# Kernel optimization log

Hardware: AMD Instinct MI355X
Metric: run time of the kernel (lower is better)

The kernel has to match this reference:

```python
import jax, jax.numpy as jnp
import numpy as np

NUM_BRANCH = 4
KERNEL_SIZES = (1, 3, 5, 7)
NUM_CLASSES = 1000
IN_C = 256
OUT_C = 256


def _cond_conv(x, w, emb, y):
    # x: [B,C,H,W], w: [O,I,k,k], emb: [num_classes,O], y: [B]
    out = jax.lax.conv_general_dilated(
        x, w, window_strides=(1, 1), padding='SAME',
        dimension_numbers=('NCHW', 'OIHW', 'NCHW'))
    return out + emb[y][:, :, None, None]


def setup_inputs() -> dict:
    key = jax.random.key(0)
    ks = jax.random.split(key, 2 + 2 * NUM_BRANCH)
    B, H = 64, 32
    inp = {
        'x': jax.random.normal(ks[0], (B, IN_C, H, H), dtype=jnp.float32),
        'y': jax.random.randint(ks[1], (B,), 0, NUM_CLASSES, dtype=jnp.int64),
        'sample_arc': jax.random.randint(jax.random.fold_in(key, 7), (B,), 0, NUM_BRANCH, dtype=jnp.int64),
    }
    for i, k in enumerate(KERNEL_SIZES):
        fan_in = IN_C * k * k
        inp[f'w{i}'] = jax.random.normal(ks[2 + 2 * i], (OUT_C, IN_C, k, k), dtype=jnp.float32) / np.sqrt(fan_in)
        inp[f'e{i}'] = jax.random.normal(ks[3 + 2 * i], (NUM_CLASSES, OUT_C), dtype=jnp.float32) * 0.02
    return inp


def reference(x, y, sample_arc, w0, w1, w2, w3, e0, e1, e2, e3):
    ws = (w0, w1, w2, w3)
    es = (e0, e1, e2, e3)
    # Compute every branch for every sample (as the original module does),
    # stack along branch dim: [B, num_branch, O, H, W]
    branch_out = jnp.stack([_cond_conv(x, w, e, y) for w, e in zip(ws, es)], axis=1)
    onehot = jax.nn.one_hot(sample_arc, NUM_BRANCH, dtype=x.dtype)  # [B, num_branch]
    # mask-and-sum (one-hot multiply then reduce over branch dim)
    return jnp.einsum('bn,bnchw->bchw', onehot, branch_out)
```

## Files before the change

### kernel.cpp

```cpp
#include <hip/hip_runtime.h>


typedef unsigned short ushort_t;
typedef __attribute__((ext_vector_type(8))) short short8;
typedef __attribute__((ext_vector_type(4))) float f32x4;

#define CIN   256
#define COUT  256
#define HH    32
#define WW    32
#define HW    1024

#define XT_ELEMS   16777216
#define WT_OFF_0   0
#define WT_OFF_1   65536
#define WT_OFF_2   655360
#define WT_OFF_3   2293760
#define WT_ELEMS   5505024
#define TILE_BYTE_OFF ((size_t)(XT_ELEMS + WT_ELEMS) * 2)
#define MAX_TILES  2048
#define WS_NEEDED  (TILE_BYTE_OFF + MAX_TILES * 2 + 64)

#define XS_R_STRIDE 1520
#define XS_C_STRIDE 40
#define XS_ELEMS    15200

__device__ inline ushort_t f2bf(float f) {
    unsigned x = __builtin_bit_cast(unsigned, f);
    unsigned r = (x + 0x7FFFu + ((x >> 16) & 1u)) >> 16;
    return (ushort_t)r;
}

__global__ __launch_bounds__(256) void prep_kernel(
    const float* __restrict__ x,
    const float* __restrict__ w0, const float* __restrict__ w1,
    const float* __restrict__ w2, const float* __restrict__ w3,
    const int* __restrict__ y, const int* __restrict__ arc,
    const float* __restrict__ e0, const float* __restrict__ e1,
    const float* __restrict__ e2, const float* __restrict__ e3,
    float* __restrict__ out,
    ushort_t* __restrict__ xt, ushort_t* __restrict__ wt,
    ushort_t* __restrict__ tiles, unsigned* __restrict__ cnt) {
    __shared__ float lds[2 * 32 * 49];
    const int blk = blockIdx.x;
    const int tid = threadIdx.x;

    if (blk < 4096) {
        const int a   = blk >> 10;
        const int cc  = (blk >> 7) & 7;
        const int oc0 = (blk & 127) * 2;
        const int kk  = (a == 0) ? 1 : (a == 1) ? 9 : (a == 2) ? 25 : 49;
        const float* __restrict__ w = (a == 0) ? w0 : (a == 1) ? w1
                                    : (a == 2) ? w2 : w3;
        const size_t woff = (a == 0) ? WT_OFF_0 : (a == 1) ? WT_OFF_1
                          : (a == 2) ? WT_OFF_2 : WT_OFF_3;
        const int ckk = 32 * kk;
#pragma unroll
        for (int ocq = 0; ocq < 2; ++ocq) {
            const float* src = w + ((size_t)((oc0 + ocq) * CIN + cc * 32)) * kk;
            for (int i = tid; i < ckk; i += 256) lds[ocq * ckk + i] = src[i];
        }
        __syncthreads();
        ushort_t* dst = wt + woff;
        const int F = 2 * kk * 32;
        for (int j = tid; j < F; j += 256) {
            const int ci  = j & 31;
            const int t2  = j >> 5;
            const int khw = t2 % kk;
            const int ocq = t2 / kk;
            dst[((size_t)(cc * kk + khw) * COUT + oc0 + ocq) * 32 + ci] =
                f2bf(lds[ocq * ckk + ci * kk + khw]);
        }
    } else if (blk < 6144) {
        const int id = (blk - 4096) * 256 + tid;
        const int hw = id & 1023;
        const int cc = (id >> 10) & 7;
        const int b  = id >> 13;
        const float* src = x + ((size_t)(b * CIN + cc * 32)) * HW + hw;
        ushort_t* dst = xt + ((size_t)((b * 8 + cc) * HW + hw)) * 32;
#pragma unroll
        for (int v = 0; v < 4; ++v) {
            short8 o;
#pragma unroll
            for (int j = 0; j < 8; ++j)
                o[j] = (short)f2bf(src[(size_t)(v * 8 + j) * HW]);
            *(short8*)(dst + v * 8) = o;
        }
    } else if (blk < 10240) {
        const int z   = blk - 6144;
        const int b   = z >> 6;
        const int oc  = (z & 63) * 4 + (tid >> 6);
        const int i   = tid & 63;
        const int a   = arc[b];
        const int cls = y[b];
        const float* __restrict__ e = (a == 0) ? e0 : (a == 1) ? e1
                                    : (a == 2) ? e2 : e3;
        const float ev = e[(size_t)cls * COUT + oc];
        float4 v = make_float4(ev, ev, ev, ev);
        float* ob = out + ((size_t)(b * COUT + oc)) * HW + i * 16;
#pragma unroll
        for (int k = 0; k < 4; ++k) *(float4*)(ob + k * 4) = v;
    } else if (tid < 64) {
        const int lane = tid;
        const int ab = (int)arc[lane];
        unsigned long long m[4];
#pragma unroll
        for (int v = 0; v < 4; ++v) m[v] = __ballot(ab == v);
        int gt = 0;
#pragma unroll
        for (int v = 1; v < 4; ++v) if (v > ab) gt += __popcll(m[v]);
        const unsigned long long eq = (ab == 0) ? m[0] : (ab == 1) ? m[1]
                                    : (ab == 2) ? m[2] : m[3];
        const unsigned long long lower = (lane == 0) ? 0ull
                                       : (~0ull >> (64 - lane));
        const int rank = gt + __popcll(eq & lower);
        const int nh   = __popcll(m[2]) + __popcll(m[3]);
        const bool heavy = (ab >= 2);
        const int myCnt = heavy ? 16 : 8;
        const int start = heavy ? 16 * rank : 16 * nh + 8 * (rank - nh);
        for (int j = 0; j < myCnt; ++j)
            tiles[start + j] = (ushort_t)((lane << 5) | j);
        if (lane == 0) { cnt[0] = 0u; cnt[1] = (unsigned)(512 + 8 * nh); }
    }
}

template <int K, int NCC, bool ATOMIC>
__device__ void conv_body(const ushort_t* __restrict__ xt,
                          const ushort_t* __restrict__ wtb,
                          const float* __restrict__ eb,
                          int b, int cls, int cc0, int r0,
                          float* __restrict__ out, ushort_t* xs) {
    constexpr int KK   = K * K;
    constexpr int PAD  = K / 2;
    constexpr int R    = 4 + 2 * PAD;
    constexpr int ITER = (R * 128) / 256;

    const int tid  = threadIdx.x;
    const int wave = tid >> 6;
    const int lane = tid & 63;
    const int wm   = wave;
    const int ln   = lane & 15;
    const int q    = lane >> 4;

    f32x4 acc[4][8];
#pragma unroll
    for (int mt = 0; mt < 4; ++mt)
#pragma unroll
        for (int nt = 0; nt < 8; ++nt) acc[mt][nt] = (f32x4)0.0f;

    constexpr size_t WSTEP = (size_t)COUT * 32;
    const ushort_t* wlane = wtb + ((size_t)(wm * 64 + ln)) * 32 + q * 8;
    short8 afp[4];
#pragma unroll
    for (int mt = 0; mt < 4; ++mt)
        afp[mt] = *(const short8*)&wlane[(size_t)(cc0 * KK) * WSTEP
                                         + (size_t)mt * 512];

    const ushort_t* xsrc = xt + ((size_t)b * 8) * (HW * 32);

    for (int cc2 = 0; cc2 < NCC; ++cc2) {
        const int cc = cc0 + cc2;
        __syncthreads();
#pragma unroll
        for (int i = 0; i < ITER; ++i) {
            const int id = tid + i * 256;
            const int r  = id >> 7;
            const int gw = (id >> 2) & 31;
            const int g4 = id & 3;
            const int gr = r0 - PAD + r;
            short8 v = (short8)0;
            if (gr >= 0 && gr < HH)
                v = *(const short8*)&xsrc[((size_t)(cc * HW + gr * WW + gw)) * 32 + g4 * 8];
            *(short8*)&xs[r * XS_R_STRIDE + (gw + 3) * XS_C_STRIDE + g4 * 8] = v;
        }
        __syncthreads();

#pragma unroll 1
        for (int kh = 0; kh < K; ++kh) {
#pragma unroll
            for (int kw = 0; kw < K; ++kw) {
                const int khw = kh * K + kw;
                const int idx = cc * KK + khw;
                short8 afc[4];
#pragma unroll
                for (int mt = 0; mt < 4; ++mt) afc[mt] = afp[mt];
                {
                    int nidx = idx + 1;
                    if (nidx == (cc0 + NCC) * KK) nidx = cc0 * KK;
                    const ushort_t* nb = wlane + (size_t)nidx * WSTEP;
#pragma unroll
                    for (int mt = 0; mt < 4; ++mt)
                        afp[mt] = *(const short8*)&nb[(size_t)mt * 512];
                }
                short8 bf[8];
#pragma unroll
                for (int nt = 0; nt < 8; ++nt) {
                    const int rl = (nt >> 1) + kh;
                    const int c  = (nt & 1) * 16 + ln + 3 + (kw - PAD);
                    bf[nt] = *(const short8*)&xs[rl * XS_R_STRIDE + c * XS_C_STRIDE + q * 8];
                }
#pragma unroll
                for (int mt = 0; mt < 4; ++mt)
#pragma unroll
                    for (int nt = 0; nt < 8; ++nt)
                        acc[mt][nt] = __builtin_amdgcn_mfma_f32_16x16x32_bf16(
                            afc[mt], bf[nt], acc[mt][nt], 0, 0, 0);
            }
        }
    }

#pragma unroll
    for (int mt = 0; mt < 4; ++mt) {
#pragma unroll
        for (int i = 0; i < 4; ++i) {
            const int oc = wm * 64 + mt * 16 + q * 4 + i;
            float* ob = out + ((size_t)(b * COUT + oc)) * HW;
            if (ATOMIC) {
#pragma unroll
                for (int nt = 0; nt < 8; ++nt) {
                    const int row = r0 + (nt >> 1);
                    const int col = (nt & 1) * 16 + ln;
                    atomicAdd(&ob[row * WW + col], acc[mt][nt][i]);
                }
            } else {
                const float ev = eb[(size_t)cls * COUT + oc];
#pragma unroll
                for (int nt = 0; nt < 8; ++nt) {
                    const int row = r0 + (nt >> 1);
                    const int col = (nt & 1) * 16 + ln;
                    ob[row * WW + col] = acc[mt][nt][i] + ev;
                }
            }
        }
    }
}

__global__ __launch_bounds__(256, 2) void conv_mfma(
    const ushort_t* __restrict__ xt, const ushort_t* __restrict__ wt,
    const int* __restrict__ y, const int* __restrict__ arc,
    const float* __restrict__ e0, const float* __restrict__ e1,
    const float* __restrict__ e2, const float* __restrict__ e3,
    float* __restrict__ out,
    const ushort_t* __restrict__ tiles, unsigned* __restrict__ cnt) {
    __shared__ ushort_t xs[XS_ELEMS];
    __shared__ int t_sh;
    const int tid = threadIdx.x;
    const unsigned T = cnt[1];

    for (int i = tid; i < 240; i += 256) {
        const int g    = i & 3;
        const int cell = i >> 2;
        const int cidx = cell % 6;
        const int r    = cell / 6;
        const int col  = (cidx < 3) ? cidx : cidx + 32;
        *(short8*)&xs[r * XS_R_STRIDE + col * XS_C_STRIDE + g * 8] = (short8)0;
    }

    for (;;) {
        if (tid == 0) {
            const unsigned t = atomicAdd(cnt, 1u);
            t_sh = (t < T) ? (int)tiles[t] : -1;
        }
        __syncthreads();
        const int e = t_sh;
        __syncthreads();
        if (e < 0) break;

        const int b   = e >> 5;
        const int j   = e & 31;
        const int a   = __builtin_amdgcn_readfirstlane(arc[b]);
        const int cls = __builtin_amdgcn_readfirstlane(y[b]);
        switch (a) {
            case 0:  conv_body<1, 8, false>(xt, wt + WT_OFF_0, e0, b, cls,
                                            0, (j & 7) << 2, out, xs); break;
            case 1:  conv_body<3, 8, false>(xt, wt + WT_OFF_1, e1, b, cls,
                                            0, (j & 7) << 2, out, xs); break;
            case 2:  conv_body<5, 4, true>(xt, wt + WT_OFF_2, e2, b, cls,
                                           (j & 1) << 2, (j >> 1) << 2, out, xs); break;
            default: conv_body<7, 4, true>(xt, wt + WT_OFF_3, e3, b, cls,
                                           (j & 1) << 2, (j >> 1) << 2, out, xs); break;
        }
    }
}

__global__ __launch_bounds__(256) void cond_conv_direct(
    const float* __restrict__ x, const int* __restrict__ y,
    const int* __restrict__ arc,
    const float* __restrict__ w0, const float* __restrict__ e0,
    const float* __restrict__ w1, const float* __restrict__ e1,
    const float* __restrict__ w2, const float* __restrict__ e2,
    const float* __restrict__ w3, const float* __restrict__ e3,
    float* __restrict__ out) {
    const int b   = blockIdx.x >> 4;
    const int o0  = (blockIdx.x & 15) << 4;
    const int tid = threadIdx.x;
    const int col  = tid & 31;
    const int row0 = tid >> 5;
    int a   = __builtin_amdgcn_readfirstlane(arc[b]);
    int cls = __builtin_amdgcn_readfirstlane(y[b]);
    const int k   = (a == 0) ? 1 : (a == 1) ? 3 : (a == 2) ? 5 : 7;
    const int kk  = k * k;
    const int pad = k >> 1;
    const float* __restrict__ wp = (a == 0) ? w0 : (a == 1) ? w1 : (a == 2) ? w2 : w3;
    const float* __restrict__ ep = (a == 0) ? e0 : (a == 1) ? e1 : (a == 2) ? e2 : e3;
    __shared__ float xsh[8 * HW];
    float acc[16][4];
#pragma unroll
    for (int o = 0; o < 16; ++o)
#pragma unroll
        for (int p = 0; p < 4; ++p) acc[o][p] = 0.f;
    const float* xb = x + (size_t)b * CIN * HW;
    for (int c0 = 0; c0 < CIN; c0 += 8) {
        __syncthreads();
        const float4* src = (const float4*)(xb + c0 * HW);
        float4* dst = (float4*)xsh;
#pragma unroll
        for (int i = 0; i < 8; ++i) dst[tid + (i << 8)] = src[tid + (i << 8)];
        __syncthreads();
        for (int kh = 0; kh < k; ++kh) {
            const int dh = kh - pad;
            int raddr[4]; bool rok[4];
#pragma unroll
            for (int p = 0; p < 4; ++p) {
                const int rr = row0 + 8 * p + dh;
                rok[p] = (rr >= 0) && (rr < HH);
                raddr[p] = (rok[p] ? rr : 0) * WW;
            }
            for (int kw = 0; kw < k; ++kw) {
                const int cc2 = col + kw - pad;
                const bool cok = (cc2 >= 0) && (cc2 < WW);
                const int cofs = cok ? cc2 : 0;
                const int khw = kh * k + kw;
#pragma unroll
                for (int ci = 0; ci < 8; ++ci) {
                    float xv[4];
#pragma unroll
                    for (int p = 0; p < 4; ++p) {
                        const float v = xsh[ci * HW + raddr[p] + cofs];
                        xv[p] = (rok[p] && cok) ? v : 0.f;
                    }
                    const float* wb = wp + (size_t)o0 * CIN * kk + (size_t)(c0 + ci) * kk + khw;
#pragma unroll
                    for (int o = 0; o < 16; ++o) {
                        const float wsv = wb[(size_t)o * CIN * kk];
#pragma unroll
                        for (int p = 0; p < 4; ++p) acc[o][p] += wsv * xv[p];
                    }
                }
            }
        }
    }
    const float* erow = ep + (size_t)cls * COUT + o0;
    float* ob = out + (size_t)(b * COUT + o0) * HW;
#pragma unroll
    for (int o = 0; o < 16; ++o) {
        const float ev = erow[o];
#pragma unroll
        for (int p = 0; p < 4; ++p)
            ob[o * HW + (row0 + 8 * p) * WW + col] = acc[o][p] + ev;
    }
}

extern "C" void kernel_launch(void* const* d_in, const int* in_sizes, int n_in,
                              void* d_out, int out_size, void* d_ws, size_t ws_size,
                              hipStream_t stream) {
    const float* x   = (const float*)d_in[0];
    const int*   y   = (const int*)  d_in[1];
    const int*   arc = (const int*)  d_in[2];
    const float* w0  = (const float*)d_in[3];
    const float* e0  = (const float*)d_in[4];
    const float* w1  = (const float*)d_in[5];
    const float* e1  = (const float*)d_in[6];
    const float* w2  = (const float*)d_in[7];
    const float* e2  = (const float*)d_in[8];
    const float* w3  = (const float*)d_in[9];
    const float* e3  = (const float*)d_in[10];
    float* out = (float*)d_out;
    const int B = in_sizes[1];

    if (ws_size >= WS_NEEDED && B == 64) {
        ushort_t* xt    = (ushort_t*)d_ws;
        ushort_t* wt    = xt + XT_ELEMS;
        ushort_t* tiles = (ushort_t*)((char*)d_ws + TILE_BYTE_OFF);
        unsigned* cnt   = (unsigned*)((char*)d_ws + TILE_BYTE_OFF + MAX_TILES * 2);
        hipLaunchKernelGGL(prep_kernel, dim3(10241), dim3(256), 0, stream,
                           x, w0, w1, w2, w3, y, arc, e0, e1, e2, e3, out,
                           xt, wt, tiles, cnt);
        hipLaunchKernelGGL(conv_mfma, dim3(512), dim3(256), 0, stream,
                           xt, wt, y, arc, e0, e1, e2, e3, out, tiles, cnt);
    } else {
        hipLaunchKernelGGL(cond_conv_direct, dim3(B * 16), dim3(256), 0, stream,
                           x, y, arc, w0, e0, w1, e1, w2, e2, w3, e3, out);
    }
}
```

Measured before the change: 427.1 us.

## Stream weight fragments into LDS via async global_load_lds triple buffer

Replaces the per-lane register prefetch of weight fragments with asynchronous global-to-LDS loads into a per-wave three-stage ring buffer, waiting on vmcnt before reading fragments from LDS. The goal is a deeper prefetch so global weight-load latency hides behind the MFMA work. The change also shrinks the input tile's LDS column stride from 40 to 32, and the prep kernel skips the embedding prefill for light branches that write their own bias. It costs extra LDS (about 48KB for weights plus a trash buffer), which may limit occupancy, and the unpadded stride may cause bank conflicts.

Result: faster. 372.0 us (-12.9%).

```diff
diff --git a/kernel.cpp b/kernel.cpp
--- a/kernel.cpp
+++ b/kernel.cpp
@@ -21,9 +21,11 @@
 #define MAX_TILES  2048
 #define WS_NEEDED  (TILE_BYTE_OFF + MAX_TILES * 2 + 64)
 
-#define XS_R_STRIDE 1520
-#define XS_C_STRIDE 40
-#define XS_ELEMS    15200
+#define XS_R_STRIDE 1216
+#define XS_C_STRIDE 32
+#define XS_ELEMS    12160
+#define WR_ELEMS    24576
+#define TRASH_ELEMS 2048
 
 __device__ inline ushort_t f2bf(float f) {
     unsigned x = __builtin_bit_cast(unsigned, f);
@@ -89,12 +91,12 @@
     } else if (blk < 10240) {
         const int z   = blk - 6144;
         const int b   = z >> 6;
+        const int a   = arc[b];
+        if (a < 2) return;
         const int oc  = (z & 63) * 4 + (tid >> 6);
         const int i   = tid & 63;
-        const int a   = arc[b];
         const int cls = y[b];
-        const float* __restrict__ e = (a == 0) ? e0 : (a == 1) ? e1
-                                    : (a == 2) ? e2 : e3;
+        const float* __restrict__ e = (a == 2) ? e2 : e3;
         const float ev = e[(size_t)cls * COUT + oc];
         float4 v = make_float4(ev, ev, ev, ev);
         float* ob = out + ((size_t)(b * COUT + oc)) * HW + i * 16;
@@ -129,7 +131,8 @@
                           const ushort_t* __restrict__ wtb,
                           const float* __restrict__ eb,
                           int b, int cls, int cc0, int r0,
-                          float* __restrict__ out, ushort_t* xs) {
+                          float* __restrict__ out,
+                          ushort_t* xs, ushort_t* wr, ushort_t* trash) {
     constexpr int KK   = K * K;
     constexpr int PAD  = K / 2;
     constexpr int R    = 4 + 2 * PAD;
@@ -138,7 +141,6 @@
     const int tid  = threadIdx.x;
     const int wave = tid >> 6;
     const int lane = tid & 63;
-    const int wm   = wave;
     const int ln   = lane & 15;
     const int q    = lane >> 4;
 
@@ -148,16 +150,28 @@
 #pragma unroll
         for (int nt = 0; nt < 8; ++nt) acc[mt][nt] = (f32x4)0.0f;
 
-    constexpr size_t WSTEP = (size_t)COUT * 32;
-    const ushort_t* wlane = wtb + ((size_t)(wm * 64 + ln)) * 32 + q * 8;
-    short8 afp[4];
-#pragma unroll
-    for (int mt = 0; mt < 4; ++mt)
-        afp[mt] = *(const short8*)&wlane[(size_t)(cc0 * KK) * WSTEP
-                                         + (size_t)mt * 512];
+    ushort_t* wrw = wr + wave * (3 * 2048);
+    const ushort_t* wsrc = wtb + (size_t)wave * 2048 + (size_t)lane * 8;
+
+    const int t0   = cc0 * KK;
+    const int TEND = (cc0 + NCC) * KK;
+
+    auto issue = [&](int idx, ushort_t* dst) {
+#pragma unroll
+        for (int mt = 0; mt < 4; ++mt)
+            __builtin_amdgcn_global_load_lds(
+                (const __attribute__((address_space(1))) void*)
+                    (wsrc + (size_t)idx * 8192 + mt * 512),
+                (__attribute__((address_space(3))) void*)
+                    (dst + mt * 512),
+                16, 0, 0);
+    };
+
+    issue(t0, wrw); issue(t0 + 1, wrw + 2048); issue(t0 + 2, wrw + 4096);
 
     const ushort_t* xsrc = xt + ((size_t)b * 8) * (HW * 32);
 
+    int rs = 0;
     for (int cc2 = 0; cc2 < NCC; ++cc2) {
         const int cc = cc0 + cc2;
         __syncthreads();
@@ -179,19 +193,17 @@
         for (int kh = 0; kh < K; ++kh) {
 #pragma unroll
             for (int kw = 0; kw < K; ++kw) {
-                const int khw = kh * K + kw;
-                const int idx = cc * KK + khw;
+                const int t = cc * KK + kh * K + kw;
+                asm volatile("s_waitcnt vmcnt(8)" ::: "memory");
+                __builtin_amdgcn_sched_barrier(0);
                 short8 afc[4];
 #pragma unroll
-                for (int mt = 0; mt < 4; ++mt) afc[mt] = afp[mt];
-                {
-                    int nidx = idx + 1;
-                    if (nidx == (cc0 + NCC) * KK) nidx = cc0 * KK;
-                    const ushort_t* nb = wlane + (size_t)nidx * WSTEP;
-#pragma unroll
-                    for (int mt = 0; mt < 4; ++mt)
-                        afp[mt] = *(const short8*)&nb[(size_t)mt * 512];
-                }
+                for (int mt = 0; mt < 4; ++mt)
+                    afc[mt] = *(const short8*)&wrw[rs * 2048 + mt * 512 + ln * 32 + q * 8];
+                asm volatile("s_waitcnt lgkmcnt(0)" ::: "memory");
+                __builtin_amdgcn_sched_barrier(0);
+                const bool real = (t + 3 < TEND);
+                issue(real ? (t + 3) : t0, real ? (wrw + rs * 2048) : trash);
                 short8 bf[8];
 #pragma unroll
                 for (int nt = 0; nt < 8; ++nt) {
@@ -205,6 +217,7 @@
                     for (int nt = 0; nt < 8; ++nt)
                         acc[mt][nt] = __builtin_amdgcn_mfma_f32_16x16x32_bf16(
                             afc[mt], bf[nt], acc[mt][nt], 0, 0, 0);
+                rs = (rs == 2) ? 0 : rs + 1;
             }
         }
     }
@@ -213,7 +226,7 @@
     for (int mt = 0; mt < 4; ++mt) {
 #pragma unroll
         for (int i = 0; i < 4; ++i) {
-            const int oc = wm * 64 + mt * 16 + q * 4 + i;
+            const int oc = wave * 64 + mt * 16 + q * 4 + i;
             float* ob = out + ((size_t)(b * COUT + oc)) * HW;
             if (ATOMIC) {
 #pragma unroll
@@ -243,6 +256,8 @@
     float* __restrict__ out,
     const ushort_t* __restrict__ tiles, unsigned* __restrict__ cnt) {
     __shared__ ushort_t xs[XS_ELEMS];
+    __shared__ ushort_t wr[WR_ELEMS];
+    __shared__ ushort_t trash[TRASH_ELEMS];
     __shared__ int t_sh;
     const int tid = threadIdx.x;
     const unsigned T = cnt[1];
@@ -272,13 +287,13 @@
         const int cls = __builtin_amdgcn_readfirstlane(y[b]);
         switch (a) {
             case 0:  conv_body<1, 8, false>(xt, wt + WT_OFF_0, e0, b, cls,
-                                            0, (j & 7) << 2, out, xs); break;
+                                            0, (j & 7) << 2, out, xs, wr, trash); break;
             case 1:  conv_body<3, 8, false>(xt, wt + WT_OFF_1, e1, b, cls,
-                                            0, (j & 7) << 2, out, xs); break;
+                                            0, (j & 7) << 2, out, xs, wr, trash); break;
             case 2:  conv_body<5, 4, true>(xt, wt + WT_OFF_2, e2, b, cls,
-                                           (j & 1) << 2, (j >> 1) << 2, out, xs); break;
+                                           (j & 1) << 2, (j >> 1) << 2, out, xs, wr, trash); break;
             default: conv_body<7, 4, true>(xt, wt + WT_OFF_3, e3, b, cls,
-                                           (j & 1) << 2, (j >> 1) << 2, out, xs); break;
+                                           (j & 1) << 2, (j >> 1) << 2, out, xs, wr, trash); break;
         }
     }
 }
```
